# Kernel tuning notes

Hardware: AMD Instinct MI355X
Metric: run time of the kernel (lower is better)

The kernel has to match this reference:

```python
import jax, jax.numpy as jnp
import numpy as np

ALPHA = 0.2  # leaky_relu negative slope


def setup_inputs() -> dict:
    key = jax.random.key(0)
    ks = jax.random.split(key, 6)
    N, E, F_IN, F_OUT, E_DIM = 50000, 800000, 256, 256, 64
    h = jax.random.normal(ks[0], (N, F_IN), dtype=jnp.float32)
    e_feat = jax.random.normal(ks[1], (E, E_DIM), dtype=jnp.float32)
    W = jax.random.normal(ks[2], (F_OUT, F_IN), dtype=jnp.float32) * (1.0 / np.sqrt(F_IN))
    A = jax.random.normal(ks[3], (1, 2 * F_OUT + E_DIM), dtype=jnp.float32) * 0.05
    src = jax.random.randint(ks[4], (E,), 0, N, dtype=jnp.int32)
    dst = jax.random.randint(ks[5], (E,), 0, N, dtype=jnp.int32)
    return {"h": h, "e_feat": e_feat, "W": W, "A": A, "src": src, "dst": dst}


def reference(h, e_feat, W, A, src, dst):
    N = h.shape[0]
    F_OUT = W.shape[0]
    # equation (1): node projection
    z = h @ W.T  # [N, F_OUT]
    z_src = z[src]  # [E, F_OUT]
    z_dst = z[dst]  # [E, F_OUT]
    # equation (2): per-edge attention logit = attn_fc([z_src, z_dst, e_feat])
    # split A to avoid materializing the [E, 2F+De] concat
    a_src, a_dst, a_e = A[0, :F_OUT], A[0, F_OUT:2 * F_OUT], A[0, 2 * F_OUT:]
    logits = z_src @ a_src + z_dst @ a_dst + e_feat @ a_e  # [E]
    e = jax.nn.leaky_relu(logits, ALPHA)
    # equations (3)&(4): segment-softmax over incoming edges per destination
    m = jax.ops.segment_max(e, dst, num_segments=N)  # [N]
    ex = jnp.exp(e - m[dst])
    denom = jax.ops.segment_sum(ex, dst, num_segments=N)  # [N]
    alpha = ex / denom[dst]  # [E]
    h_out = jax.ops.segment_sum(alpha[:, None] * z_src, dst, num_segments=N)
    return h_out
```

## Files before the change

### kernel.cpp

```cpp
#include <hip/hip_runtime.h>
#include <hip/hip_bf16.h>

#define FDIM 256
#define EDIM 64
#define LEAKY 0.2f

#define BM 64
#define BK 32

#define SCAN_BLOCKS 64

typedef __attribute__((ext_vector_type(8))) short bfrag;
typedef __attribute__((ext_vector_type(4))) float f4acc;

__device__ __forceinline__ unsigned f2bf(float x){
    unsigned u = __float_as_uint(x);
    return (u + 0x7FFFu + ((u >> 16) & 1u)) >> 16;
}
__device__ __forceinline__ float bf2f(unsigned b){
    return __uint_as_float(b << 16);
}
__device__ __forceinline__ unsigned pack_hi(float x, float y, float& hx, float& hy){
    unsigned bx = f2bf(x), by = f2bf(y);
    hx = bf2f(bx); hy = bf2f(by);
    return bx | (by << 16);
}
__device__ __forceinline__ unsigned pack_lo(float rx, float ry){
    return f2bf(rx) | (f2bf(ry) << 16);
}

__device__ __forceinline__ void gbar(int* bar, int idx, int nb){
    __syncthreads();
    if (threadIdx.x == 0){
        __threadfence();
        atomicAdd(&bar[idx], 1);
        while (__hip_atomic_load(&bar[idx], __ATOMIC_ACQUIRE, __HIP_MEMORY_SCOPE_AGENT) < nb){}
        __threadfence();
    }
    __syncthreads();
}

__global__ void k_prep(const float* __restrict__ W, unsigned short* __restrict__ W16,
                       const int* __restrict__ dst, int* __restrict__ counts,
                       int* __restrict__ bar, int E){
    int gt = blockIdx.x*256 + threadIdx.x;
    if (gt == 0){ bar[0] = 0; bar[1] = 0; }
    if (gt < (FDIM*FDIM)/4){
        int i = gt*4;
        float4 v = *(const float4*)&W[i];
        uint2 o;
        o.x = f2bf(v.x) | (f2bf(v.y) << 16);
        o.y = f2bf(v.z) | (f2bf(v.w) << 16);
        *(uint2*)&W16[i] = o;
    }
    if (gt < E) atomicAdd(&counts[dst[gt]], 1);
}

__global__ __launch_bounds__(256, 3) void k_gemm(const float* __restrict__ h,
                                                 const unsigned short* __restrict__ W16,
                                                 const float* __restrict__ A,
                                                 unsigned short* __restrict__ z16,
                                                 float* __restrict__ s_src,
                                                 float* __restrict__ s_dst, int M){
    __shared__ uint4 smA[BM*8];
    __shared__ uint4 smB[FDIM*8];
    __shared__ float sred[4][2][BM];

    int tid = threadIdx.x;
    int m0 = blockIdx.x * BM;

    int wid  = tid >> 6;
    int lane = tid & 63;
    int wn = wid * 64;
    int l15 = lane & 15;
    int l4  = lane >> 4;

    f4acc acc[4][4];
    #pragma unroll
    for (int i = 0; i < 4; ++i)
        #pragma unroll
        for (int j = 0; j < 4; ++j)
            acc[i][j] = (f4acc)(0.f);

    for (int kc = 0; kc < FDIM; kc += BK){
        {
            int row = tid >> 2, k8 = tid & 3;
            int gr = m0 + row;
            float4 v0, v1;
            if (gr < M){
                const float* g = &h[(size_t)gr*FDIM + kc + k8*8];
                v0 = *(const float4*)g; v1 = *(const float4*)(g + 4);
            } else {
                v0 = make_float4(0.f,0.f,0.f,0.f); v1 = v0;
            }
            uint4 hi, lo; float hx, hy;
            hi.x = pack_hi(v0.x, v0.y, hx, hy);
            lo.x = pack_lo(v0.x - hx, v0.y - hy);
            hi.y = pack_hi(v0.z, v0.w, hx, hy);
            lo.y = pack_lo(v0.z - hx, v0.w - hy);
            hi.z = pack_hi(v1.x, v1.y, hx, hy);
            lo.z = pack_lo(v1.x - hx, v1.y - hy);
            hi.w = pack_hi(v1.z, v1.w, hx, hy);
            lo.w = pack_lo(v1.z - hx, v1.w - hy);
            int sh = k8 ^ (row & 7);
            smA[row*8 + sh]       = hi;
            smA[row*8 + (sh ^ 4)] = lo;
        }
        #pragma unroll
        for (int q = 0; q < 4; ++q){
            int p = tid + q*256;
            int row = p >> 2, k8 = p & 3;
            uint4 v = *(const uint4*)&W16[(size_t)row*FDIM + kc + k8*8];
            smB[row*8 + (k8 ^ (row & 7))] = v;
        }
        __syncthreads();

        bfrag ah[4], al[4];
        #pragma unroll
        for (int mf = 0; mf < 4; ++mf){
            int row = mf*16 + l15;
            int sh = l4 ^ (row & 7);
            ah[mf] = *(const bfrag*)&smA[row*8 + sh];
            al[mf] = *(const bfrag*)&smA[row*8 + (sh ^ 4)];
        }
        #pragma unroll
        for (int nf = 0; nf < 4; ++nf){
            int row = wn + nf*16 + l15;
            bfrag bh = *(const bfrag*)&smB[row*8 + (l4 ^ (row & 7))];
            #pragma unroll
            for (int mf = 0; mf < 4; ++mf){
                acc[mf][nf] = __builtin_amdgcn_mfma_f32_16x16x32_bf16(ah[mf], bh, acc[mf][nf], 0, 0, 0);
                acc[mf][nf] = __builtin_amdgcn_mfma_f32_16x16x32_bf16(al[mf], bh, acc[mf][nf], 0, 0, 0);
            }
        }
        __syncthreads();
    }

    #pragma unroll
    for (int mf = 0; mf < 4; ++mf){
        #pragma unroll
        for (int nf = 0; nf < 4; ++nf){
            int gcol = wn + nf*16 + l15;
            #pragma unroll
            for (int r = 0; r < 4; ++r){
                int grow = m0 + mf*16 + l4*4 + r;
                if (grow < M)
                    z16[(size_t)grow*FDIM + gcol] = (unsigned short)f2bf(acc[mf][nf][r]);
            }
        }
    }

    float aS[4], aD[4];
    #pragma unroll
    for (int nf = 0; nf < 4; ++nf){
        int gcol = wn + nf*16 + l15;
        aS[nf] = A[gcol];
        aD[nf] = A[FDIM + gcol];
    }
    #pragma unroll
    for (int mf = 0; mf < 4; ++mf){
        #pragma unroll
        for (int r = 0; r < 4; ++r){
            float ps = 0.f, pd = 0.f;
            #pragma unroll
            for (int nf = 0; nf < 4; ++nf){
                ps += acc[mf][nf][r] * aS[nf];
                pd += acc[mf][nf][r] * aD[nf];
            }
            #pragma unroll
            for (int o = 1; o < 16; o <<= 1){
                ps += __shfl_xor(ps, o);
                pd += __shfl_xor(pd, o);
            }
            if (l15 == 0){
                int row = mf*16 + l4*4 + r;
                sred[wid][0][row] = ps;
                sred[wid][1][row] = pd;
            }
        }
    }
    __syncthreads();
    if (tid < BM){
        int grow = m0 + tid;
        if (grow < M){
            s_src[grow] = (sred[0][0][tid] + sred[1][0][tid]) + (sred[2][0][tid] + sred[3][0][tid]);
            s_dst[grow] = (sred[0][1][tid] + sred[1][1][tid]) + (sred[2][1][tid] + sred[3][1][tid]);
        }
    }
}

__global__ __launch_bounds__(256) void k_scan(int* __restrict__ counts, int* __restrict__ cursor,
                                              int* __restrict__ bsums, int* __restrict__ bar,
                                              int N, int E){
    __shared__ int sh[256];
    int tid = threadIdx.x;
    int chunk = (N + SCAN_BLOCKS - 1) / SCAN_BLOCKS;
    int c0 = blockIdx.x * chunk;
    int lim = min(c0 + chunk, N);

    int s = 0;
    for (int i = c0 + tid; i < lim; i += 256) s += counts[i];
    sh[tid] = s; __syncthreads();
    for (int o = 128; o > 0; o >>= 1){
        if (tid < o) sh[tid] += sh[tid + o];
        __syncthreads();
    }
    if (tid == 0) bsums[blockIdx.x] = sh[0];

    gbar(bar, 0, SCAN_BLOCKS);

    if (blockIdx.x == 0 && tid < 64){
        int v = bsums[tid];
        int orig = v;
        #pragma unroll
        for (int o = 1; o < 64; o <<= 1){
            int t = __shfl_up(v, o);
            if (tid >= o) v += t;
        }
        bsums[tid] = v - orig;
    }

    gbar(bar, 1, SCAN_BLOCKS);

    int base = c0 + tid*4;
    int v[4]; int ts = 0;
    #pragma unroll
    for (int l = 0; l < 4; l++){
        int idx = base + l;
        v[l] = (idx < lim) ? counts[idx] : 0;
        ts += v[l];
    }
    __syncthreads();
    sh[tid] = ts; __syncthreads();
    int acc = ts;
    for (int o = 1; o < 256; o <<= 1){
        int t = (tid >= o) ? sh[tid - o] : 0;
        __syncthreads();
        acc += t; sh[tid] = acc;
        __syncthreads();
    }
    int excl = acc - ts + bsums[blockIdx.x];
    #pragma unroll
    for (int l = 0; l < 4; l++){
        int idx = base + l;
        if (idx < lim){ counts[idx] = excl; cursor[idx] = excl; }
        excl += v[l];
    }
    if (blockIdx.x == 0 && tid == 0) counts[N] = E;
}

__global__ void k_edge(const float* __restrict__ ef, const float* __restrict__ A,
                       const float* __restrict__ s_src, const float* __restrict__ s_dst,
                       const int* __restrict__ src, const int* __restrict__ dst,
                       int* __restrict__ cursor, int2* __restrict__ epair, int E){
    int gt = blockIdx.x*256 + threadIdx.x;
    int e = gt >> 4, l4 = gt & 15;
    if (e >= E) return;
    float4 f  = *(const float4*)&ef[(size_t)e*EDIM + l4*4];
    float4 ae = *(const float4*)&A[2*FDIM + l4*4];
    float v = f.x*ae.x + f.y*ae.y + f.z*ae.z + f.w*ae.w;
    v += __shfl_xor(v, 8); v += __shfl_xor(v, 4);
    v += __shfl_xor(v, 2); v += __shfl_xor(v, 1);
    if (l4 == 0){
        int d = dst[e];
        float lg = v + s_src[src[e]] + s_dst[d];
        lg = lg > 0.f ? lg : LEAKY*lg;
        int p = atomicAdd(&cursor[d], 1);
        int2 pr; pr.x = src[e]; pr.y = __float_as_int(lg);
        epair[p] = pr;
    }
}

__global__ __launch_bounds__(256) void k_out(const unsigned short* __restrict__ z16,
                                             const int* __restrict__ offsets,
                                             const int2* __restrict__ epair,
                                             float* __restrict__ out, int N){
    int n = blockIdx.x*4 + (threadIdx.x >> 6);
    int lane = threadIdx.x & 63;
    if (n >= N) return;
    int i0 = offsets[n], i1 = offsets[n+1];

    float mlane = -3.402823466e38f;
    for (int i = i0 + lane; i < i1; i += 64)
        mlane = fmaxf(mlane, __int_as_float(epair[i].y));
    float mx = mlane;
    #pragma unroll
    for (int o = 32; o > 0; o >>= 1)
        mx = fmaxf(mx, __shfl_xor(mx, o));

    float4 a[4];
    a[0] = make_float4(0,0,0,0); a[1] = a[0]; a[2] = a[0]; a[3] = a[0];
    float dw = 0.f;
    const unsigned short* zb = z16 + lane*4;

    for (int base = i0; base < i1; base += 64){
        int cnt = min(64, i1 - base);
        int2 pe = make_int2(0, 0);
        float w = 0.f;
        if (lane < cnt){
            pe = epair[base + lane];
            w = __expf(__int_as_float(pe.y) - mx);
        }
        dw += w;
        int j = 0;
        for (; j + 7 < cnt; j += 8){
            float wj[8]; int sj[8]; uint2 rj[8];
            #pragma unroll
            for (int q = 0; q < 8; ++q){
                wj[q] = __shfl(w, j + q);
                sj[q] = __shfl(pe.x, j + q);
            }
            #pragma unroll
            for (int q = 0; q < 8; ++q)
                rj[q] = *(const uint2*)&zb[(size_t)sj[q]*FDIM];
            #pragma unroll
            for (int q = 0; q < 8; ++q){
                a[q & 3].x += wj[q]*bf2f(rj[q].x & 0xffffu);
                a[q & 3].y += wj[q]*bf2f(rj[q].x >> 16);
                a[q & 3].z += wj[q]*bf2f(rj[q].y & 0xffffu);
                a[q & 3].w += wj[q]*bf2f(rj[q].y >> 16);
            }
        }
        for (; j < cnt; ++j){
            float wq = __shfl(w, j);
            int   sq = __shfl(pe.x, j);
            uint2 r0 = *(const uint2*)&zb[(size_t)sq*FDIM];
            a[0].x += wq*bf2f(r0.x & 0xffffu);
            a[0].y += wq*bf2f(r0.x >> 16);
            a[0].z += wq*bf2f(r0.y & 0xffffu);
            a[0].w += wq*bf2f(r0.y >> 16);
        }
    }

    #pragma unroll
    for (int o = 32; o > 0; o >>= 1)
        dw += __shfl_xor(dw, o);

    float inv = (i1 > i0) ? 1.f / dw : 0.f;
    float4 res;
    res.x = ((a[0].x + a[1].x) + (a[2].x + a[3].x)) * inv;
    res.y = ((a[0].y + a[1].y) + (a[2].y + a[3].y)) * inv;
    res.z = ((a[0].z + a[1].z) + (a[2].z + a[3].z)) * inv;
    res.w = ((a[0].w + a[1].w) + (a[2].w + a[3].w)) * inv;
    *(float4*)&out[(size_t)n*FDIM + lane*4] = res;
}

extern "C" void kernel_launch(void* const* d_in, const int* in_sizes, int n_in,
                              void* d_out, int out_size, void* d_ws, size_t ws_size,
                              hipStream_t stream){
    const float* h  = (const float*)d_in[0];
    const float* ef = (const float*)d_in[1];
    const float* W  = (const float*)d_in[2];
    const float* A  = (const float*)d_in[3];
    const int*  src = (const int*)d_in[4];
    const int*  dst = (const int*)d_in[5];
    float* out = (float*)d_out;
    int N = in_sizes[0] / FDIM;
    int E = in_sizes[4];

    char* ws = (char*)d_ws;
    size_t off = 0;
    auto alloc = [&](size_t nbytes)->char*{
        char* p = ws + off;
        off = (off + nbytes + 255) & ~(size_t)255;
        return p;
    };
    unsigned short* z16 = (unsigned short*)alloc((size_t)N*FDIM*2);
    unsigned short* W16 = (unsigned short*)alloc((size_t)FDIM*FDIM*2);
    float* s_src  = (float*)alloc((size_t)N*4);
    float* s_dst  = (float*)alloc((size_t)N*4);
    int*   counts = (int*)alloc((size_t)(N+1)*4);
    int*   cursor = (int*)alloc((size_t)N*4);
    int2*  epair  = (int2*)alloc((size_t)E*8);
    int*   bsums  = (int*)alloc(SCAN_BLOCKS*4);
    int*   bar    = (int*)alloc(2*4);

    hipMemsetAsync(counts, 0, (size_t)(N+1)*4, stream);
    hipLaunchKernelGGL(k_prep, dim3((E+255)/256), dim3(256), 0, stream,
                       W, W16, dst, counts, bar, E);
    hipLaunchKernelGGL(k_gemm, dim3((N+BM-1)/BM), dim3(256), 0, stream,
                       h, W16, A, z16, s_src, s_dst, N);
    hipLaunchKernelGGL(k_scan, dim3(SCAN_BLOCKS), dim3(256), 0, stream,
                       counts, cursor, bsums, bar, N, E);
    hipLaunchKernelGGL(k_edge, dim3((E+15)/16), dim3(256), 0, stream,
                       ef, A, s_src, s_dst, src, dst, cursor, epair, E);
    hipLaunchKernelGGL(k_out, dim3((N+3)/4), dim3(256), 0, stream,
                       z16, counts, epair, out, N);
}
```

Measured before the change: 238.8 us.

## Fuse edge-feature dot and degree count into GEMM launch, enlarge GEMM tile

The edge-feature dot product and the destination-degree histogram move out of the prep and edge kernels into extra blocks of the GEMM launch. They now run concurrently with the node projection, and the dot result goes to an edot buffer. The GEMM tile grows to 128x256 with a 2x2 warp layout, so the bf16 weights are loaded into LDS half as often per row. The later edge kernel becomes one thread per edge that reads edot. This adds an E-sized float buffer round trip and a larger register footprint in exchange for overlapping the memory-bound edge-feature stream with the GEMM.

```diff
diff --git a/kernel.cpp b/kernel.cpp
--- a/kernel.cpp
+++ b/kernel.cpp
@@ -5,7 +5,8 @@
 #define EDIM 64
 #define LEAKY 0.2f
 
-#define BM 64
+#define BM 128
+#define BN 256
 #define BK 32
 
 #define SCAN_BLOCKS 64
@@ -40,91 +41,112 @@
     __syncthreads();
 }
 
-__global__ void k_prep(const float* __restrict__ W, unsigned short* __restrict__ W16,
-                       const int* __restrict__ dst, int* __restrict__ counts,
-                       int* __restrict__ bar, int E){
+__global__ void k_wconv(const float* __restrict__ W, unsigned short* __restrict__ W16,
+                        int* __restrict__ bar){
     int gt = blockIdx.x*256 + threadIdx.x;
     if (gt == 0){ bar[0] = 0; bar[1] = 0; }
-    if (gt < (FDIM*FDIM)/4){
-        int i = gt*4;
-        float4 v = *(const float4*)&W[i];
-        uint2 o;
-        o.x = f2bf(v.x) | (f2bf(v.y) << 16);
-        o.y = f2bf(v.z) | (f2bf(v.w) << 16);
-        *(uint2*)&W16[i] = o;
-    }
-    if (gt < E) atomicAdd(&counts[dst[gt]], 1);
-}
-
-__global__ __launch_bounds__(256, 3) void k_gemm(const float* __restrict__ h,
+    int i = gt*4;
+    float4 v = *(const float4*)&W[i];
+    uint2 o;
+    o.x = f2bf(v.x) | (f2bf(v.y) << 16);
+    o.y = f2bf(v.z) | (f2bf(v.w) << 16);
+    *(uint2*)&W16[i] = o;
+}
+
+__global__ __launch_bounds__(256, 2) void k_mega(const float* __restrict__ h,
                                                  const unsigned short* __restrict__ W16,
                                                  const float* __restrict__ A,
                                                  unsigned short* __restrict__ z16,
                                                  float* __restrict__ s_src,
-                                                 float* __restrict__ s_dst, int M){
+                                                 float* __restrict__ s_dst, int M, int nGemm,
+                                                 const float* __restrict__ ef,
+                                                 const int* __restrict__ dst,
+                                                 float* __restrict__ edot,
+                                                 int* __restrict__ counts, int E){
     __shared__ uint4 smA[BM*8];
-    __shared__ uint4 smB[FDIM*8];
-    __shared__ float sred[4][2][BM];
+    __shared__ uint4 smB[BN*8];
+    __shared__ float sred[2][2][BM];
 
     int tid = threadIdx.x;
+
+    if ((int)blockIdx.x >= nGemm){
+        int bid = blockIdx.x - nGemm;
+        int e = bid*16 + (tid >> 4);
+        int l4 = tid & 15;
+        if (e < E){
+            float4 f  = *(const float4*)&ef[(size_t)e*EDIM + l4*4];
+            float4 ae = *(const float4*)&A[2*FDIM + l4*4];
+            float v = f.x*ae.x + f.y*ae.y + f.z*ae.z + f.w*ae.w;
+            v += __shfl_xor(v, 8); v += __shfl_xor(v, 4);
+            v += __shfl_xor(v, 2); v += __shfl_xor(v, 1);
+            if (l4 == 0){
+                edot[e] = v;
+                atomicAdd(&counts[dst[e]], 1);
+            }
+        }
+        return;
+    }
+
     int m0 = blockIdx.x * BM;
-
     int wid  = tid >> 6;
     int lane = tid & 63;
-    int wn = wid * 64;
+    int wm = (wid >> 1) * 64;
+    int wn = (wid & 1) * 128;
     int l15 = lane & 15;
     int l4  = lane >> 4;
 
-    f4acc acc[4][4];
+    f4acc acc[4][8];
     #pragma unroll
     for (int i = 0; i < 4; ++i)
         #pragma unroll
-        for (int j = 0; j < 4; ++j)
+        for (int j = 0; j < 8; ++j)
             acc[i][j] = (f4acc)(0.f);
 
     for (int kc = 0; kc < FDIM; kc += BK){
-        {
-            int row = tid >> 2, k8 = tid & 3;
-            int gr = m0 + row;
-            float4 v0, v1;
-            if (gr < M){
-                const float* g = &h[(size_t)gr*FDIM + kc + k8*8];
-                v0 = *(const float4*)g; v1 = *(const float4*)(g + 4);
+        #pragma unroll
+        for (int q = 0; q < 6; ++q){
+            int p = tid + q*256;
+            if (p < 512){
+                int row = p >> 2, k8 = p & 3;
+                int gr = m0 + row;
+                float4 v0, v1;
+                if (gr < M){
+                    const float* g = &h[(size_t)gr*FDIM + kc + k8*8];
+                    v0 = *(const float4*)g; v1 = *(const float4*)(g + 4);
+                } else {
+                    v0 = make_float4(0.f,0.f,0.f,0.f); v1 = v0;
+                }
+                uint4 hi, lo; float hx, hy;
+                hi.x = pack_hi(v0.x, v0.y, hx, hy);
+                lo.x = pack_lo(v0.x - hx, v0.y - hy);
+                hi.y = pack_hi(v0.z, v0.w, hx, hy);
+                lo.y = pack_lo(v0.z - hx, v0.w - hy);
+                hi.z = pack_hi(v1.x, v1.y, hx, hy);
+                lo.z = pack_lo(v1.x - hx, v1.y - hy);
+                hi.w = pack_hi(v1.z, v1.w, hx, hy);
+                lo.w = pack_lo(v1.z - hx, v1.w - hy);
+                int sh = k8 ^ (row & 7);
+                smA[row*8 + sh]       = hi;
+                smA[row*8 + (sh ^ 4)] = lo;
             } else {
-                v0 = make_float4(0.f,0.f,0.f,0.f); v1 = v0;
-            }
-            uint4 hi, lo; float hx, hy;
-            hi.x = pack_hi(v0.x, v0.y, hx, hy);
-            lo.x = pack_lo(v0.x - hx, v0.y - hy);
-            hi.y = pack_hi(v0.z, v0.w, hx, hy);
-            lo.y = pack_lo(v0.z - hx, v0.w - hy);
-            hi.z = pack_hi(v1.x, v1.y, hx, hy);
-            lo.z = pack_lo(v1.x - hx, v1.y - hy);
-            hi.w = pack_hi(v1.z, v1.w, hx, hy);
-            lo.w = pack_lo(v1.z - hx, v1.w - hy);
-            int sh = k8 ^ (row & 7);
-            smA[row*8 + sh]       = hi;
-            smA[row*8 + (sh ^ 4)] = lo;
-        }
-        #pragma unroll
-        for (int q = 0; q < 4; ++q){
-            int p = tid + q*256;
-            int row = p >> 2, k8 = p & 3;
-            uint4 v = *(const uint4*)&W16[(size_t)row*FDIM + kc + k8*8];
-            smB[row*8 + (k8 ^ (row & 7))] = v;
+                int pb = p - 512;
+                int row = pb >> 2, k8 = pb & 3;
+                uint4 v = *(const uint4*)&W16[(size_t)row*FDIM + kc + k8*8];
+                smB[row*8 + (k8 ^ (row & 7))] = v;
+            }
         }
         __syncthreads();
 
         bfrag ah[4], al[4];
         #pragma unroll
         for (int mf = 0; mf < 4; ++mf){
-            int row = mf*16 + l15;
+            int row = wm + mf*16 + l15;
             int sh = l4 ^ (row & 7);
             ah[mf] = *(const bfrag*)&smA[row*8 + sh];
             al[mf] = *(const bfrag*)&smA[row*8 + (sh ^ 4)];
         }
         #pragma unroll
-        for (int nf = 0; nf < 4; ++nf){
+        for (int nf = 0; nf < 8; ++nf){
             int row = wn + nf*16 + l15;
             bfrag bh = *(const bfrag*)&smB[row*8 + (l4 ^ (row & 7))];
             #pragma unroll
@@ -139,20 +161,20 @@
     #pragma unroll
     for (int mf = 0; mf < 4; ++mf){
         #pragma unroll
-        for (int nf = 0; nf < 4; ++nf){
+        for (int nf = 0; nf < 8; ++nf){
             int gcol = wn + nf*16 + l15;
             #pragma unroll
             for (int r = 0; r < 4; ++r){
-                int grow = m0 + mf*16 + l4*4 + r;
+                int grow = m0 + wm + mf*16 + l4*4 + r;
                 if (grow < M)
                     z16[(size_t)grow*FDIM + gcol] = (unsigned short)f2bf(acc[mf][nf][r]);
             }
         }
     }
 
-    float aS[4], aD[4];
-    #pragma unroll
-    for (int nf = 0; nf < 4; ++nf){
+    float aS[8], aD[8];
+    #pragma unroll
+    for (int nf = 0; nf < 8; ++nf){
         int gcol = wn + nf*16 + l15;
         aS[nf] = A[gcol];
         aD[nf] = A[FDIM + gcol];
@@ -163,7 +185,7 @@
         for (int r = 0; r < 4; ++r){
             float ps = 0.f, pd = 0.f;
             #pragma unroll
-            for (int nf = 0; nf < 4; ++nf){
+            for (int nf = 0; nf < 8; ++nf){
                 ps += acc[mf][nf][r] * aS[nf];
                 pd += acc[mf][nf][r] * aD[nf];
             }
@@ -173,9 +195,9 @@
                 pd += __shfl_xor(pd, o);
             }
             if (l15 == 0){
-                int row = mf*16 + l4*4 + r;
-                sred[wid][0][row] = ps;
-                sred[wid][1][row] = pd;
+                int row = wm + mf*16 + l4*4 + r;
+                sred[wid & 1][0][row] = ps;
+                sred[wid & 1][1][row] = pd;
             }
         }
     }
@@ -183,8 +205,8 @@
     if (tid < BM){
         int grow = m0 + tid;
         if (grow < M){
-            s_src[grow] = (sred[0][0][tid] + sred[1][0][tid]) + (sred[2][0][tid] + sred[3][0][tid]);
-            s_dst[grow] = (sred[0][1][tid] + sred[1][1][tid]) + (sred[2][1][tid] + sred[3][1][tid]);
+            s_src[grow] = sred[0][0][tid] + sred[1][0][tid];
+            s_dst[grow] = sred[0][1][tid] + sred[1][1][tid];
         }
     }
 }
@@ -249,26 +271,18 @@
     if (blockIdx.x == 0 && tid == 0) counts[N] = E;
 }
 
-__global__ void k_edge(const float* __restrict__ ef, const float* __restrict__ A,
-                       const float* __restrict__ s_src, const float* __restrict__ s_dst,
-                       const int* __restrict__ src, const int* __restrict__ dst,
-                       int* __restrict__ cursor, int2* __restrict__ epair, int E){
-    int gt = blockIdx.x*256 + threadIdx.x;
-    int e = gt >> 4, l4 = gt & 15;
+__global__ void k_edge2(const float* __restrict__ edot,
+                        const float* __restrict__ s_src, const float* __restrict__ s_dst,
+                        const int* __restrict__ src, const int* __restrict__ dst,
+                        int* __restrict__ cursor, int2* __restrict__ epair, int E){
+    int e = blockIdx.x*256 + threadIdx.x;
     if (e >= E) return;
-    float4 f  = *(const float4*)&ef[(size_t)e*EDIM + l4*4];
-    float4 ae = *(const float4*)&A[2*FDIM + l4*4];
-    float v = f.x*ae.x + f.y*ae.y + f.z*ae.z + f.w*ae.w;
-    v += __shfl_xor(v, 8); v += __shfl_xor(v, 4);
-    v += __shfl_xor(v, 2); v += __shfl_xor(v, 1);
-    if (l4 == 0){
-        int d = dst[e];
-        float lg = v + s_src[src[e]] + s_dst[d];
-        lg = lg > 0.f ? lg : LEAKY*lg;
-        int p = atomicAdd(&cursor[d], 1);
-        int2 pr; pr.x = src[e]; pr.y = __float_as_int(lg);
-        epair[p] = pr;
-    }
+    int sN = src[e], dN = dst[e];
+    float lg = edot[e] + s_src[sN] + s_dst[dN];
+    lg = lg > 0.f ? lg : LEAKY*lg;
+    int p = atomicAdd(&cursor[dN], 1);
+    int2 pr; pr.x = sN; pr.y = __float_as_int(lg);
+    epair[p] = pr;
 }
 
 __global__ __launch_bounds__(256) void k_out(const unsigned short* __restrict__ z16,
@@ -369,21 +383,25 @@
     unsigned short* W16 = (unsigned short*)alloc((size_t)FDIM*FDIM*2);
     float* s_src  = (float*)alloc((size_t)N*4);
     float* s_dst  = (float*)alloc((size_t)N*4);
+    float* edot   = (float*)alloc((size_t)E*4);
     int*   counts = (int*)alloc((size_t)(N+1)*4);
     int*   cursor = (int*)alloc((size_t)N*4);
     int2*  epair  = (int2*)alloc((size_t)E*8);
     int*   bsums  = (int*)alloc(SCAN_BLOCKS*4);
     int*   bar    = (int*)alloc(2*4);
 
+    int nGemm = (N + BM - 1) / BM;
+    int nEf   = (E + 15) / 16;
+
     hipMemsetAsync(counts, 0, (size_t)(N+1)*4, stream);
-    hipLaunchKernelGGL(k_prep, dim3((E+255)/256), dim3(256), 0, stream,
-                       W, W16, dst, counts, bar, E);
-    hipLaunchKernelGGL(k_gemm, dim3((N+BM-1)/BM), dim3(256), 0, stream,
-                       h, W16, A, z16, s_src, s_dst, N);
+    hipLaunchKernelGGL(k_wconv, dim3(64), dim3(256), 0, stream, W, W16, bar);
+    hipLaunchKernelGGL(k_mega, dim3(nGemm + nEf), dim3(256), 0, stream,
+                       h, W16, A, z16, s_src, s_dst, N, nGemm,
+                       ef, dst, edot, counts, E);
     hipLaunchKernelGGL(k_scan, dim3(SCAN_BLOCKS), dim3(256), 0, stream,
                        counts, cursor, bsums, bar, N, E);
-    hipLaunchKernelGGL(k_edge, dim3((E+15)/16), dim3(256), 0, stream,
-                       ef, A, s_src, s_dst, src, dst, cursor, epair, E);
+    hipLaunchKernelGGL(k_edge2, dim3((E+255)/256), dim3(256), 0, stream,
+                       edot, s_src, s_dst, src, dst, cursor, epair, E);
     hipLaunchKernelGGL(k_out, dim3((N+3)/4), dim3(256), 0, stream,
                        z16, counts, epair, out, N);
 }
```

Result: slower. 305.3 us (+27.8%).

## Enlarge GEMM tile to 128 rows and load W directly into LDS

Applied to the files above, without the earlier changes.

Doubles the node-projection GEMM row tile to 128 and arranges the four waves as 2x2, each computing a 64x128 sub-tile, so every W tile staged in shared memory is reused across twice as many rows. The bf16 W tile is now brought in with global_load_lds direct-to-LDS transfers instead of going through registers. Twice as many accumulator registers are needed, so occupancy is lowered to 2 blocks per SM. The grid is also halved, which may leave fewer blocks to balance across CUs.

```diff
diff --git a/kernel.cpp b/kernel.cpp
--- a/kernel.cpp
+++ b/kernel.cpp
@@ -5,7 +5,8 @@
 #define EDIM 64
 #define LEAKY 0.2f
 
-#define BM 64
+#define BM 128
+#define BN 256
 #define BK 32
 
 #define SCAN_BLOCKS 64
@@ -27,6 +28,12 @@
 }
 __device__ __forceinline__ unsigned pack_lo(float rx, float ry){
     return f2bf(rx) | (f2bf(ry) << 16);
+}
+
+__device__ __forceinline__ void gload16(void* lds, const void* g){
+    __builtin_amdgcn_global_load_lds(
+        (const __attribute__((address_space(1))) unsigned int*)g,
+        (__attribute__((address_space(3))) unsigned int*)lds, 16, 0, 0);
 }
 
 __device__ __forceinline__ void gbar(int* bar, int idx, int nb){
@@ -56,35 +63,46 @@
     if (gt < E) atomicAdd(&counts[dst[gt]], 1);
 }
 
-__global__ __launch_bounds__(256, 3) void k_gemm(const float* __restrict__ h,
+__global__ __launch_bounds__(256, 2) void k_gemm(const float* __restrict__ h,
                                                  const unsigned short* __restrict__ W16,
                                                  const float* __restrict__ A,
                                                  unsigned short* __restrict__ z16,
                                                  float* __restrict__ s_src,
                                                  float* __restrict__ s_dst, int M){
     __shared__ uint4 smA[BM*8];
-    __shared__ uint4 smB[FDIM*8];
-    __shared__ float sred[4][2][BM];
+    __shared__ uint4 smB[BN*8];
+    __shared__ float sred[2][2][BM];
 
     int tid = threadIdx.x;
     int m0 = blockIdx.x * BM;
 
     int wid  = tid >> 6;
     int lane = tid & 63;
-    int wn = wid * 64;
+    int wm = (wid >> 1) * 64;
+    int wn = (wid & 1) * 128;
     int l15 = lane & 15;
     int l4  = lane >> 4;
 
-    f4acc acc[4][4];
+    f4acc acc[4][8];
     #pragma unroll
     for (int i = 0; i < 4; ++i)
         #pragma unroll
-        for (int j = 0; j < 4; ++j)
+        for (int j = 0; j < 8; ++j)
             acc[i][j] = (f4acc)(0.f);
 
     for (int kc = 0; kc < FDIM; kc += BK){
-        {
-            int row = tid >> 2, k8 = tid & 3;
+        #pragma unroll
+        for (int q = 0; q < 8; ++q){
+            int s = tid + q*256;
+            int row = s >> 3;
+            int k8 = (s & 7) ^ (row & 7);
+            const unsigned short* g = &W16[(size_t)row*FDIM + kc + (k8 & 3)*8];
+            gload16(&smB[s], g);
+        }
+        #pragma unroll
+        for (int q = 0; q < 2; ++q){
+            int p = tid + q*256;
+            int row = p >> 2, k8 = p & 3;
             int gr = m0 + row;
             float4 v0, v1;
             if (gr < M){
@@ -106,25 +124,18 @@
             smA[row*8 + sh]       = hi;
             smA[row*8 + (sh ^ 4)] = lo;
         }
-        #pragma unroll
-        for (int q = 0; q < 4; ++q){
-            int p = tid + q*256;
-            int row = p >> 2, k8 = p & 3;
-            uint4 v = *(const uint4*)&W16[(size_t)row*FDIM + kc + k8*8];
-            smB[row*8 + (k8 ^ (row & 7))] = v;
-        }
         __syncthreads();
 
         bfrag ah[4], al[4];
         #pragma unroll
         for (int mf = 0; mf < 4; ++mf){
-            int row = mf*16 + l15;
+            int row = wm + mf*16 + l15;
             int sh = l4 ^ (row & 7);
             ah[mf] = *(const bfrag*)&smA[row*8 + sh];
             al[mf] = *(const bfrag*)&smA[row*8 + (sh ^ 4)];
         }
         #pragma unroll
-        for (int nf = 0; nf < 4; ++nf){
+        for (int nf = 0; nf < 8; ++nf){
             int row = wn + nf*16 + l15;
             bfrag bh = *(const bfrag*)&smB[row*8 + (l4 ^ (row & 7))];
             #pragma unroll
@@ -139,20 +150,20 @@
     #pragma unroll
     for (int mf = 0; mf < 4; ++mf){
         #pragma unroll
-        for (int nf = 0; nf < 4; ++nf){
+        for (int nf = 0; nf < 8; ++nf){
             int gcol = wn + nf*16 + l15;
             #pragma unroll
             for (int r = 0; r < 4; ++r){
-                int grow = m0 + mf*16 + l4*4 + r;
+                int grow = m0 + wm + mf*16 + l4*4 + r;
                 if (grow < M)
                     z16[(size_t)grow*FDIM + gcol] = (unsigned short)f2bf(acc[mf][nf][r]);
             }
         }
     }
 
-    float aS[4], aD[4];
-    #pragma unroll
-    for (int nf = 0; nf < 4; ++nf){
+    float aS[8], aD[8];
+    #pragma unroll
+    for (int nf = 0; nf < 8; ++nf){
         int gcol = wn + nf*16 + l15;
         aS[nf] = A[gcol];
         aD[nf] = A[FDIM + gcol];
@@ -163,7 +174,7 @@
         for (int r = 0; r < 4; ++r){
             float ps = 0.f, pd = 0.f;
             #pragma unroll
-            for (int nf = 0; nf < 4; ++nf){
+            for (int nf = 0; nf < 8; ++nf){
                 ps += acc[mf][nf][r] * aS[nf];
                 pd += acc[mf][nf][r] * aD[nf];
             }
@@ -173,9 +184,9 @@
                 pd += __shfl_xor(pd, o);
             }
             if (l15 == 0){
-                int row = mf*16 + l4*4 + r;
-                sred[wid][0][row] = ps;
-                sred[wid][1][row] = pd;
+                int row = wm + mf*16 + l4*4 + r;
+                sred[wid & 1][0][row] = ps;
+                sred[wid & 1][1][row] = pd;
             }
         }
     }
@@ -183,8 +194,8 @@
     if (tid < BM){
         int grow = m0 + tid;
         if (grow < M){
-            s_src[grow] = (sred[0][0][tid] + sred[1][0][tid]) + (sred[2][0][tid] + sred[3][0][tid]);
-            s_dst[grow] = (sred[0][1][tid] + sred[1][1][tid]) + (sred[2][1][tid] + sred[3][1][tid]);
+            s_src[grow] = sred[0][0][tid] + sred[1][0][tid];
+            s_dst[grow] = sred[0][1][tid] + sred[1][1][tid];
         }
     }
 }
```

Measured after the change: 233.6 us. 1.02x faster.

## Enlarge GEMM block tile to 128 rows with 8 waves in a 2x4 layout

Applied to the files above, without the earlier changes.

The projection GEMM now uses 512-thread blocks covering 128 rows of h. Eight waves are laid out as 2 along M by 4 along N. The shared W tile is compacted to 4 uint4 slots per row with a new XOR swizzle, and B fragments are loaded once and reused across the M fragments. This aims to halve the number of W tile loads per output row and cut shared-memory footprint, at the cost of larger blocks with fewer of them and possible register pressure under launch_bounds(512,4).

```diff
diff --git a/kernel.cpp b/kernel.cpp
--- a/kernel.cpp
+++ b/kernel.cpp
@@ -5,7 +5,8 @@
 #define EDIM 64
 #define LEAKY 0.2f
 
-#define BM 64
+#define BM 128
+#define BN 256
 #define BK 32
 
 #define SCAN_BLOCKS 64
@@ -56,14 +57,14 @@
     if (gt < E) atomicAdd(&counts[dst[gt]], 1);
 }
 
-__global__ __launch_bounds__(256, 3) void k_gemm(const float* __restrict__ h,
+__global__ __launch_bounds__(512, 4) void k_gemm(const float* __restrict__ h,
                                                  const unsigned short* __restrict__ W16,
                                                  const float* __restrict__ A,
                                                  unsigned short* __restrict__ z16,
                                                  float* __restrict__ s_src,
                                                  float* __restrict__ s_dst, int M){
     __shared__ uint4 smA[BM*8];
-    __shared__ uint4 smB[FDIM*8];
+    __shared__ uint4 smB[BN*4];
     __shared__ float sred[4][2][BM];
 
     int tid = threadIdx.x;
@@ -71,7 +72,8 @@
 
     int wid  = tid >> 6;
     int lane = tid & 63;
-    int wn = wid * 64;
+    int wm = (wid >> 2) * 64;
+    int wn = (wid & 3) * 64;
     int l15 = lane & 15;
     int l4  = lane >> 4;
 
@@ -107,30 +109,32 @@
             smA[row*8 + (sh ^ 4)] = lo;
         }
         #pragma unroll
-        for (int q = 0; q < 4; ++q){
-            int p = tid + q*256;
+        for (int q = 0; q < 2; ++q){
+            int p = tid + q*512;
             int row = p >> 2, k8 = p & 3;
             uint4 v = *(const uint4*)&W16[(size_t)row*FDIM + kc + k8*8];
-            smB[row*8 + (k8 ^ (row & 7))] = v;
-        }
-        __syncthreads();
-
-        bfrag ah[4], al[4];
-        #pragma unroll
-        for (int mf = 0; mf < 4; ++mf){
-            int row = mf*16 + l15;
-            int sh = l4 ^ (row & 7);
-            ah[mf] = *(const bfrag*)&smA[row*8 + sh];
-            al[mf] = *(const bfrag*)&smA[row*8 + (sh ^ 4)];
-        }
+            int sw = (k8 ^ row ^ (row >> 2)) & 3;
+            smB[row*4 + sw] = v;
+        }
+        __syncthreads();
+
+        bfrag bhv[4];
         #pragma unroll
         for (int nf = 0; nf < 4; ++nf){
             int row = wn + nf*16 + l15;
-            bfrag bh = *(const bfrag*)&smB[row*8 + (l4 ^ (row & 7))];
-            #pragma unroll
-            for (int mf = 0; mf < 4; ++mf){
-                acc[mf][nf] = __builtin_amdgcn_mfma_f32_16x16x32_bf16(ah[mf], bh, acc[mf][nf], 0, 0, 0);
-                acc[mf][nf] = __builtin_amdgcn_mfma_f32_16x16x32_bf16(al[mf], bh, acc[mf][nf], 0, 0, 0);
+            int sw = (l4 ^ row ^ (row >> 2)) & 3;
+            bhv[nf] = *(const bfrag*)&smB[row*4 + sw];
+        }
+        #pragma unroll
+        for (int mf = 0; mf < 4; ++mf){
+            int row = wm + mf*16 + l15;
+            int sh = l4 ^ (row & 7);
+            bfrag ah = *(const bfrag*)&smA[row*8 + sh];
+            bfrag al = *(const bfrag*)&smA[row*8 + (sh ^ 4)];
+            #pragma unroll
+            for (int nf = 0; nf < 4; ++nf){
+                acc[mf][nf] = __builtin_amdgcn_mfma_f32_16x16x32_bf16(ah, bhv[nf], acc[mf][nf], 0, 0, 0);
+                acc[mf][nf] = __builtin_amdgcn_mfma_f32_16x16x32_bf16(al, bhv[nf], acc[mf][nf], 0, 0, 0);
             }
         }
         __syncthreads();
@@ -143,7 +147,7 @@
             int gcol = wn + nf*16 + l15;
             #pragma unroll
             for (int r = 0; r < 4; ++r){
-                int grow = m0 + mf*16 + l4*4 + r;
+                int grow = m0 + wm + mf*16 + l4*4 + r;
                 if (grow < M)
                     z16[(size_t)grow*FDIM + gcol] = (unsigned short)f2bf(acc[mf][nf][r]);
             }
@@ -173,9 +177,9 @@
                 pd += __shfl_xor(pd, o);
             }
             if (l15 == 0){
-                int row = mf*16 + l4*4 + r;
-                sred[wid][0][row] = ps;
-                sred[wid][1][row] = pd;
+                int row = wm + mf*16 + l4*4 + r;
+                sred[wid & 3][0][row] = ps;
+                sred[wid & 3][1][row] = pd;
             }
         }
     }
@@ -378,7 +382,7 @@
     hipMemsetAsync(counts, 0, (size_t)(N+1)*4, stream);
     hipLaunchKernelGGL(k_prep, dim3((E+255)/256), dim3(256), 0, stream,
                        W, W16, dst, counts, bar, E);
-    hipLaunchKernelGGL(k_gemm, dim3((N+BM-1)/BM), dim3(256), 0, stream,
+    hipLaunchKernelGGL(k_gemm, dim3((N+BM-1)/BM), dim3(512), 0, stream,
                        h, W16, A, z16, s_src, s_dst, N);
     hipLaunchKernelGGL(k_scan, dim3(SCAN_BLOCKS), dim3(256), 0, stream,
                        counts, cursor, bsums, bar, N, E);
```

Measured after the change: 237.8 us. No clear change (-0.4%).
